# Performance work log

Measured on AMD Instinct MI355X. Metric: run time of the kernel, lower is better.

The kernel has to match this reference:

```python
import jax, jax.numpy as jnp
import numpy as np

CUTOFF = 5.0
N_RBF = 50
N_INTER = 6
B = 1024          # molecules per batch
N_PER_MOL = 32    # atoms per molecule
MAX_Z = 100
D = 128           # n_atom_basis == n_filters == head_hidden


def _ssp(x):
    # schnetpack shifted softplus activation
    return jax.nn.softplus(x) - jnp.log(2.0).astype(x.dtype)


def setup_inputs() -> dict:
    key = jax.random.key(0)
    ks = jax.random.split(key, 18)
    total = B * N_PER_MOL
    atomic_numbers = jax.random.randint(ks[0], (total,), 1, MAX_Z, dtype=jnp.int32)
    positions = jax.random.uniform(ks[1], (total, 3), dtype=jnp.float32) * 10.0
    # all ordered intra-molecule pairs with i != j; pairs beyond the cutoff are
    # zeroed by the cosine cutoff factor, matching the torch neighbor-list math
    loc = np.arange(N_PER_MOL)
    ii, jj = np.meshgrid(loc, loc, indexing='ij')
    m = ii != jj
    li, lj = ii[m], jj[m]                      # [n*(n-1)]
    off = (np.arange(B) * N_PER_MOL)[:, None]
    idx_i = jnp.asarray((off + li[None, :]).reshape(-1), dtype=jnp.int32)
    idx_j = jnp.asarray((off + lj[None, :]).reshape(-1), dtype=jnp.int32)
    batch_idx = jnp.asarray(np.repeat(np.arange(B), N_PER_MOL), dtype=jnp.int32)
    n_atoms = jnp.full((B,), N_PER_MOL, dtype=jnp.int32)
    s = 0.05
    emb = jax.random.normal(ks[2], (MAX_Z, D), jnp.float32) * s
    Wi  = jax.random.normal(ks[3], (N_INTER, D, D), jnp.float32) * s      # in2f (no bias)
    Wf1 = jax.random.normal(ks[4], (N_INTER, N_RBF, D), jnp.float32) * s  # filter net
    bf1 = jax.random.normal(ks[5], (N_INTER, D), jnp.float32) * s
    Wf2 = jax.random.normal(ks[6], (N_INTER, D, D), jnp.float32) * s
    bf2 = jax.random.normal(ks[7], (N_INTER, D), jnp.float32) * s
    Wo1 = jax.random.normal(ks[8], (N_INTER, D, D), jnp.float32) * s      # f2out
    bo1 = jax.random.normal(ks[9], (N_INTER, D), jnp.float32) * s
    Wo2 = jax.random.normal(ks[10], (N_INTER, D, D), jnp.float32) * s
    bo2 = jax.random.normal(ks[11], (N_INTER, D), jnp.float32) * s
    Wh1 = jax.random.normal(ks[12], (D, D), jnp.float32) * s              # MLP head
    bh1 = jax.random.normal(ks[13], (D,), jnp.float32) * s
    Wh2 = jax.random.normal(ks[14], (D, 1), jnp.float32) * s
    bh2 = jax.random.normal(ks[15], (1,), jnp.float32) * s
    return dict(atomic_numbers=atomic_numbers, positions=positions, idx_i=idx_i,
                idx_j=idx_j, batch_idx=batch_idx, n_atoms=n_atoms, emb=emb,
                Wi=Wi, Wf1=Wf1, bf1=bf1, Wf2=Wf2, bf2=bf2,
                Wo1=Wo1, bo1=bo1, Wo2=Wo2, bo2=bo2,
                Wh1=Wh1, bh1=bh1, Wh2=Wh2, bh2=bh2)


def reference(atomic_numbers, positions, idx_i, idx_j, batch_idx, n_atoms,
              emb, Wi, Wf1, bf1, Wf2, bf2, Wo1, bo1, Wo2, bo2,
              Wh1, bh1, Wh2, bh2):
    total = atomic_numbers.shape[0]
    nmol = n_atoms.shape[0]
    # pairwise displacement / distance over neighbor list
    Rij = positions[idx_j] - positions[idx_i]                    # [P,3]
    d = jnp.sqrt(jnp.sum(Rij * Rij, axis=-1))                    # [P]
    # GaussianRBF: centers on [0, cutoff], width = spacing
    centers = jnp.linspace(0.0, CUTOFF, N_RBF, dtype=d.dtype)
    width = CUTOFF / (N_RBF - 1)
    coeff = -0.5 / (width * width)
    f_ij = jnp.exp(coeff * (d[:, None] - centers[None, :]) ** 2)  # [P,R]
    # CosineCutoff (zero beyond cutoff -> out-of-range pairs contribute nothing)
    rcut = 0.5 * (jnp.cos(d * jnp.pi / CUTOFF) + 1.0) * (d < CUTOFF)  # [P]
    x = emb[atomic_numbers]                                       # [N,D]
    for l in range(N_INTER):
        W = _ssp(f_ij @ Wf1[l] + bf1[l]) @ Wf2[l] + bf2[l]        # [P,D] filters
        W = W * rcut[:, None]
        xf = x @ Wi[l]                                            # in2f, no bias
        msg = xf[idx_j] * W                                       # gather + modulate
        agg = jax.ops.segment_sum(msg, idx_i, num_segments=total) # scatter-add
        v = _ssp(agg @ Wo1[l] + bo1[l]) @ Wo2[l] + bo2[l]         # f2out
        x = x + v                                                 # residual
    mol = jax.ops.segment_sum(x, batch_idx, num_segments=nmol)    # sum pooling
    h = jax.nn.silu(mol @ Wh1 + bh1)
    pred = (h @ Wh2 + bh2)[:, 0]                                  # squeeze(-1)
    return pred
```

## Files before the change

kernel.cpp:

```cpp
#include <hip/hip_runtime.h>
#include <math.h>

#define TOTAL  32768
#define NMOL   1024
#define NA     32
#define DIM    128
#define NRBF   50
#define NLAYER 6

typedef __attribute__((ext_vector_type(16))) float f32x16;
typedef _Float16 h2 __attribute__((ext_vector_type(2)));
typedef __fp16 hf8 __attribute__((ext_vector_type(8)));

#define OFF_TAB  0
#define OFF_XBAG 29376
#define OFF_XF   46784
#define OFF_POS  46784
#define OFF_CM   64192
#define LDS_TOTAL 81600

#define WS_WIT   0
#define WS_WO1T  196608
#define WS_WO2T  393216
#define WS_TAB   655360

#define KSTEP  0.10204081632653061f
#define C1     -48.0200005f
#define NTAB   172
#define TSCALE 34.2f

__device__ __forceinline__ unsigned pk2_f16(float lo, float hi) {
  return __builtin_bit_cast(unsigned, __builtin_amdgcn_cvt_pkrtz(lo, hi));
}
__device__ __forceinline__ float ssp_f(float v) {
  float e = __expf(-fabsf(v));
  return fmaxf(v, 0.0f) + __logf(1.0f + e) - 0.69314718055994531f;
}
__device__ __forceinline__ hf8 ldsH(const char* p) {
  return __builtin_bit_cast(hf8, *reinterpret_cast<const uint4*>(p));
}
__device__ __forceinline__ hf8 asH(uint4 u) {
  return __builtin_bit_cast(hf8, u);
}
__device__ __forceinline__ int inv_partner(int r, int i) {
  if (i == 31) return r;
  int mm = i - r; if (mm < 0) mm += 31;
  if (mm == 0) return 31;
  int jj = 2 * r - i; jj %= 31; if (jj < 0) jj += 31;
  return jj;
}

__global__ void k_prep(const float* __restrict__ Wi, const float* __restrict__ Wo1,
                       const float* __restrict__ Wo2, short* __restrict__ ws) {
  const int kind = blockIdx.y, l = blockIdx.z;
  const int idx = blockIdx.x * 256 + threadIdx.x;
  int k = idx >> 7, c = idx & 127;
  const float* s = (kind == 0) ? Wi : (kind == 1) ? Wo1 : Wo2;
  size_t base = (kind == 0) ? WS_WIT : (kind == 1) ? WS_WO1T : WS_WO2T;
  float v = s[(size_t)l * DIM * DIM + k * DIM + c];
  ws[base / 2 + (size_t)l * 16384 + (k >> 3) * 1024 + c * 8 + (k & 7)] =
      (short)__builtin_bit_cast(unsigned short, (_Float16)v);
}

__global__ void k_tab(const float* __restrict__ Wf1, const float* __restrict__ bf1,
                      const float* __restrict__ Wf2, const float* __restrict__ bf2,
                      short* __restrict__ tab) {
  __shared__ float fs[64];
  __shared__ float hs[128];
  const int g = blockIdx.x, l = blockIdx.y, c = threadIdx.x;
  const float d = (float)g * (5.0f / 171.0f);
  if (c < NRBF) { float tt = d - (float)c * KSTEP; fs[c] = __expf(C1 * tt * tt); }
  __syncthreads();
  float h = bf1[l * DIM + c];
#pragma unroll 5
  for (int k = 0; k < NRBF; ++k) h += fs[k] * Wf1[((size_t)l * NRBF + k) * DIM + c];
  hs[c] = ssp_f(h);
  __syncthreads();
  float wv = bf2[l * DIM + c];
#pragma unroll 8
  for (int k = 0; k < DIM; ++k) wv += hs[k] * Wf2[((size_t)l * DIM + k) * DIM + c];
  tab[((size_t)l * NTAB + g) * 136 + c] =
      (short)__builtin_bit_cast(unsigned short, (_Float16)wv);
}

__global__ __launch_bounds__(512, 4) void k_fused(
    const int* __restrict__ z, const float* __restrict__ pos,
    const float* __restrict__ emb,
    const short* __restrict__ wiT, const short* __restrict__ wo1T,
    const short* __restrict__ wo2T, const short* __restrict__ tabA,
    const float* __restrict__ bo1, const float* __restrict__ bo2,
    const float* __restrict__ Wh1, const float* __restrict__ bh1,
    const float* __restrict__ Wh2, const float* __restrict__ bh2,
    float* __restrict__ out) {
  extern __shared__ char sm[];
  const int t = threadIdx.x;
  const int bid = blockIdx.x;
  const int w = t >> 6, lane = t & 63, hl = lane >> 5, lr = lane & 31;
  const int m = w >> 2, wl = w & 3;
  const int ai = t & 31;
  const int acg = (t >> 5) & 7;
  const int cgo = acg * 16;

  char*  XBm = sm + OFF_XBAG + m * 8704;
  char*  AGm = XBm;
  char*  XFm = sm + OFF_XF + m * 8704;
  float* poss = (float*)(sm + OFF_POS);
  const char* CMm = sm + OFF_CM + m * 8704;

  if (t < 192) poss[t] = pos[(size_t)bid * 192 + t];
  __syncthreads();
  for (int u = t; u < 2048; u += 512) {
    int m2 = u >> 10, e = u & 1023;
    int r = e >> 5, i = e & 31;
    uint2 me;
    if (r < 31) {
      int j = inv_partner(r, i);
      const float* pm = poss + m2 * 96;
      float dx = pm[j * 3 + 0] - pm[i * 3 + 0];
      float dy = pm[j * 3 + 1] - pm[i * 3 + 1];
      float dz = pm[j * 3 + 2] - pm[i * 3 + 2];
      float d = sqrtf(dx * dx + dy * dy + dz * dz);
      float rc = 0.5f * (__cosf(d * 0.62831853071795865f) + 1.0f);
      rc = (d < 5.0f) ? rc : 0.0f;
      float u0 = fminf(d * TSCALE, 170.0f);
      int g = (int)u0;
      float f = u0 - (float)g;
      me.x = ((unsigned)(g * 272) << 16) | (unsigned)(j * 272);
      me.y = pk2_f16((1.0f - f) * rc, f * rc);
    } else {
      me.x = 0u; me.y = 0u;
    }
    *(uint2*)(sm + OFF_CM + m2 * 8704 + i * 272 + r * 8) = me;
  }
  float xr[16];
  {
    const float* er = emb + (size_t)z[(bid * 2 + m) * NA + ai] * DIM;
    float4 e0 = *(const float4*)&er[acg * 8];
    float4 e1 = *(const float4*)&er[acg * 8 + 4];
    float4 e2 = *(const float4*)&er[64 + acg * 8];
    float4 e3 = *(const float4*)&er[64 + acg * 8 + 4];
    xr[0] = e0.x; xr[1] = e0.y; xr[2]  = e0.z; xr[3]  = e0.w;
    xr[4] = e1.x; xr[5] = e1.y; xr[6]  = e1.z; xr[7]  = e1.w;
    xr[8] = e2.x; xr[9] = e2.y; xr[10] = e2.z; xr[11] = e2.w;
    xr[12] = e3.x; xr[13] = e3.y; xr[14] = e3.z; xr[15] = e3.w;
  }
  __syncthreads();

  uint4 pt0, pt1, pt2, pt3, pt4, pt5;

  for (int l = 0; l < NLAYER; ++l) {
    const short* wiL  = wiT  + (size_t)l * 16384;
    const short* wo1L = wo1T + (size_t)l * 16384;
    const short* wo2L = wo2T + (size_t)l * 16384;
    const short* tabL = tabA + (size_t)l * NTAB * 136;
    const float bo1r = bo1[l * DIM + wl * 32 + lr];
    const float bo2r = bo2[l * DIM + wl * 32 + lr];
    const int col = wl * 32 + lr;

    if (l > 0) {
      uint4 v0 = *(const uint4*)(XFm + ai * 272 + cgo);
      uint4 v1 = *(const uint4*)(XFm + ai * 272 + cgo + 128);
      h2 hv;
      hv = __builtin_bit_cast(h2, v0.x); xr[0]  += (float)hv[0]; xr[1]  += (float)hv[1];
      hv = __builtin_bit_cast(h2, v0.y); xr[2]  += (float)hv[0]; xr[3]  += (float)hv[1];
      hv = __builtin_bit_cast(h2, v0.z); xr[4]  += (float)hv[0]; xr[5]  += (float)hv[1];
      hv = __builtin_bit_cast(h2, v0.w); xr[6]  += (float)hv[0]; xr[7]  += (float)hv[1];
      hv = __builtin_bit_cast(h2, v1.x); xr[8]  += (float)hv[0]; xr[9]  += (float)hv[1];
      hv = __builtin_bit_cast(h2, v1.y); xr[10] += (float)hv[0]; xr[11] += (float)hv[1];
      hv = __builtin_bit_cast(h2, v1.z); xr[12] += (float)hv[0]; xr[13] += (float)hv[1];
      hv = __builtin_bit_cast(h2, v1.w); xr[14] += (float)hv[0]; xr[15] += (float)hv[1];
    }
    {
      uint4 s0, s1;
      s0.x = pk2_f16(xr[0], xr[1]);   s0.y = pk2_f16(xr[2], xr[3]);
      s0.z = pk2_f16(xr[4], xr[5]);   s0.w = pk2_f16(xr[6], xr[7]);
      s1.x = pk2_f16(xr[8], xr[9]);   s1.y = pk2_f16(xr[10], xr[11]);
      s1.z = pk2_f16(xr[12], xr[13]); s1.w = pk2_f16(xr[14], xr[15]);
      *(uint4*)(XBm + ai * 272 + cgo) = s0;
      *(uint4*)(XBm + ai * 272 + cgo + 128) = s1;
    }
    {
      const uint4* s4 = (const uint4*)tabL;
      pt0 = s4[t]; pt1 = s4[t + 512]; pt2 = s4[t + 1024];
      pt3 = s4[t + 1536]; pt4 = s4[t + 2048];
      if (t < 364) pt5 = s4[t + 2560];
    }
    __syncthreads();

    {
      uint4 bf[8];
#pragma unroll
      for (int ks = 0; ks < 8; ++ks)
        bf[ks] = *(const uint4*)(wiL + (ks * 2 + hl) * 1024 + col * 8);
      f32x16 acc;
#pragma unroll
      for (int q = 0; q < 16; ++q) acc[q] = 0.0f;
#pragma unroll
      for (int ks = 0; ks < 8; ++ks) {
        hf8 a = ldsH(XBm + lr * 272 + ks * 32 + hl * 16);
        acc = __builtin_amdgcn_mfma_f32_32x32x16_f16(a, asH(bf[ks]), acc, 0, 0, 0);
      }
#pragma unroll
      for (int rg = 0; rg < 16; rg += 2) {
        int row = (rg & 3) + 8 * (rg >> 2) + 4 * hl;
        unsigned pk = pk2_f16(acc[rg], acc[rg + 1]);
        *(unsigned short*)(XFm + row * 272 + col * 2) = (unsigned short)pk;
        *(unsigned short*)(XFm + (row + 1) * 272 + col * 2) = (unsigned short)(pk >> 16);
      }
    }
    __syncthreads();

    ((uint4*)(sm + OFF_TAB))[t] = pt0;
    ((uint4*)(sm + OFF_TAB))[t + 512] = pt1;
    ((uint4*)(sm + OFF_TAB))[t + 1024] = pt2;
    ((uint4*)(sm + OFF_TAB))[t + 1536] = pt3;
    ((uint4*)(sm + OFF_TAB))[t + 2048] = pt4;
    if (t < 364) ((uint4*)(sm + OFF_TAB))[t + 2560] = pt5;
    __syncthreads();

    h2 acc_h[8];
#pragma unroll
    for (int q = 0; q < 8; ++q) acc_h[q] = (h2)(_Float16)0.0f;
#pragma unroll 2
    for (int k = 0; k < 16; ++k) {
      uint4 ME = *(const uint4*)(CMm + ai * 272 + k * 16);
#define AGROUND(mex, mey)                                                 \
      {                                                                   \
        int foff = (int)((mex) & 0xFFFFu);                                \
        int gboff = (int)((mex) >> 16);                                   \
        unsigned a = (mey);                                               \
        h2 a00h = __builtin_bit_cast(h2, __builtin_amdgcn_perm(a, a, 0x01000100u)); \
        h2 a11h = __builtin_bit_cast(h2, __builtin_amdgcn_perm(a, a, 0x03020302u)); \
        const char* tp = sm + OFF_TAB + gboff + cgo;                      \
        uint4 T00 = *(const uint4*)(tp);                                  \
        uint4 T01 = *(const uint4*)(tp + 128);                            \
        uint4 T10 = *(const uint4*)(tp + 272);                            \
        uint4 T11 = *(const uint4*)(tp + 400);                            \
        const char* fp = XFm + foff + cgo;                                \
        uint4 F0 = *(const uint4*)(fp);                                   \
        uint4 F1 = *(const uint4*)(fp + 128);                             \
        h2 wv;                                                            \
        wv = a00h * __builtin_bit_cast(h2, T00.x) + a11h * __builtin_bit_cast(h2, T10.x); \
        acc_h[0] = wv * __builtin_bit_cast(h2, F0.x) + acc_h[0];          \
        wv = a00h * __builtin_bit_cast(h2, T00.y) + a11h * __builtin_bit_cast(h2, T10.y); \
        acc_h[1] = wv * __builtin_bit_cast(h2, F0.y) + acc_h[1];          \
        wv = a00h * __builtin_bit_cast(h2, T00.z) + a11h * __builtin_bit_cast(h2, T10.z); \
        acc_h[2] = wv * __builtin_bit_cast(h2, F0.z) + acc_h[2];          \
        wv = a00h * __builtin_bit_cast(h2, T00.w) + a11h * __builtin_bit_cast(h2, T10.w); \
        acc_h[3] = wv * __builtin_bit_cast(h2, F0.w) + acc_h[3];          \
        wv = a00h * __builtin_bit_cast(h2, T01.x) + a11h * __builtin_bit_cast(h2, T11.x); \
        acc_h[4] = wv * __builtin_bit_cast(h2, F1.x) + acc_h[4];          \
        wv = a00h * __builtin_bit_cast(h2, T01.y) + a11h * __builtin_bit_cast(h2, T11.y); \
        acc_h[5] = wv * __builtin_bit_cast(h2, F1.y) + acc_h[5];          \
        wv = a00h * __builtin_bit_cast(h2, T01.z) + a11h * __builtin_bit_cast(h2, T11.z); \
        acc_h[6] = wv * __builtin_bit_cast(h2, F1.z) + acc_h[6];          \
        wv = a00h * __builtin_bit_cast(h2, T01.w) + a11h * __builtin_bit_cast(h2, T11.w); \
        acc_h[7] = wv * __builtin_bit_cast(h2, F1.w) + acc_h[7];          \
      }
      AGROUND(ME.x, ME.y)
      AGROUND(ME.z, ME.w)
#undef AGROUND
    }
    __syncthreads();

    {
      uint4 s0, s1;
      s0.x = __builtin_bit_cast(unsigned, acc_h[0]);
      s0.y = __builtin_bit_cast(unsigned, acc_h[1]);
      s0.z = __builtin_bit_cast(unsigned, acc_h[2]);
      s0.w = __builtin_bit_cast(unsigned, acc_h[3]);
      s1.x = __builtin_bit_cast(unsigned, acc_h[4]);
      s1.y = __builtin_bit_cast(unsigned, acc_h[5]);
      s1.z = __builtin_bit_cast(unsigned, acc_h[6]);
      s1.w = __builtin_bit_cast(unsigned, acc_h[7]);
      *(uint4*)(AGm + ai * 272 + cgo) = s0;
      *(uint4*)(AGm + ai * 272 + cgo + 128) = s1;
    }
    __syncthreads();

    float t1v[16];
    {
      uint4 bf[8];
#pragma unroll
      for (int ks = 0; ks < 8; ++ks)
        bf[ks] = *(const uint4*)(wo1L + (ks * 2 + hl) * 1024 + col * 8);
      f32x16 acc;
#pragma unroll
      for (int q = 0; q < 16; ++q) acc[q] = 0.0f;
#pragma unroll
      for (int ks = 0; ks < 8; ++ks) {
        hf8 a = ldsH(AGm + lr * 272 + ks * 32 + hl * 16);
        acc = __builtin_amdgcn_mfma_f32_32x32x16_f16(a, asH(bf[ks]), acc, 0, 0, 0);
      }
#pragma unroll
      for (int rg = 0; rg < 16; ++rg) t1v[rg] = ssp_f(acc[rg] + bo1r);
    }
    __syncthreads();

    {
#pragma unroll
      for (int rg = 0; rg < 16; rg += 2) {
        int row = (rg & 3) + 8 * (rg >> 2) + 4 * hl;
        unsigned pk = pk2_f16(t1v[rg], t1v[rg + 1]);
        *(unsigned short*)(AGm + row * 272 + col * 2) = (unsigned short)pk;
        *(unsigned short*)(AGm + (row + 1) * 272 + col * 2) = (unsigned short)(pk >> 16);
      }
    }
    __syncthreads();

    {
      uint4 bf[8];
#pragma unroll
      for (int ks = 0; ks < 8; ++ks)
        bf[ks] = *(const uint4*)(wo2L + (ks * 2 + hl) * 1024 + col * 8);
      f32x16 acc;
#pragma unroll
      for (int q = 0; q < 16; ++q) acc[q] = 0.0f;
#pragma unroll
      for (int ks = 0; ks < 8; ++ks) {
        hf8 a = ldsH(AGm + lr * 272 + ks * 32 + hl * 16);
        acc = __builtin_amdgcn_mfma_f32_32x32x16_f16(a, asH(bf[ks]), acc, 0, 0, 0);
      }
#pragma unroll
      for (int rg = 0; rg < 16; rg += 2) {
        int row = (rg & 3) + 8 * (rg >> 2) + 4 * hl;
        unsigned pk = pk2_f16(acc[rg] + bo2r, acc[rg + 1] + bo2r);
        *(unsigned short*)(XFm + row * 272 + col * 2) = (unsigned short)pk;
        *(unsigned short*)(XFm + (row + 1) * 272 + col * 2) = (unsigned short)(pk >> 16);
      }
    }
    __syncthreads();
  }

  {
    uint4 v0 = *(const uint4*)(XFm + ai * 272 + cgo);
    uint4 v1 = *(const uint4*)(XFm + ai * 272 + cgo + 128);
    h2 hv;
    hv = __builtin_bit_cast(h2, v0.x); xr[0]  += (float)hv[0]; xr[1]  += (float)hv[1];
    hv = __builtin_bit_cast(h2, v0.y); xr[2]  += (float)hv[0]; xr[3]  += (float)hv[1];
    hv = __builtin_bit_cast(h2, v0.z); xr[4]  += (float)hv[0]; xr[5]  += (float)hv[1];
    hv = __builtin_bit_cast(h2, v0.w); xr[6]  += (float)hv[0]; xr[7]  += (float)hv[1];
    hv = __builtin_bit_cast(h2, v1.x); xr[8]  += (float)hv[0]; xr[9]  += (float)hv[1];
    hv = __builtin_bit_cast(h2, v1.y); xr[10] += (float)hv[0]; xr[11] += (float)hv[1];
    hv = __builtin_bit_cast(h2, v1.z); xr[12] += (float)hv[0]; xr[13] += (float)hv[1];
    hv = __builtin_bit_cast(h2, v1.w); xr[14] += (float)hv[0]; xr[15] += (float)hv[1];
  }

#pragma unroll
  for (int off = 1; off < 32; off <<= 1) {
#pragma unroll
    for (int q = 0; q < 16; ++q) xr[q] += __shfl_xor(xr[q], off);
  }
  float* molS = (float*)(sm + 0);
  float* hsum = (float*)(sm + 2048);
  if (ai == 0) {
#pragma unroll
    for (int q = 0; q < 8; ++q) molS[m * 132 + acg * 8 + q] = xr[q];
#pragma unroll
    for (int q = 0; q < 8; ++q) molS[m * 132 + 64 + acg * 8 + q] = xr[8 + q];
  }
  __syncthreads();
  if (t < 256) {
    int mm = t >> 7, c = t & 127;
    float h = bh1[c];
#pragma unroll 8
    for (int k = 0; k < 128; ++k) h += molS[mm * 132 + k] * Wh1[k * 128 + c];
    h = h / (1.0f + __expf(-h));
    hsum[mm * 128 + c] = h * Wh2[c];
  }
  for (int off = 64; off > 0; off >>= 1) {
    __syncthreads();
    if (t < 256) {
      int mm = t >> 7, c = t & 127;
      if (c < off) hsum[mm * 128 + c] += hsum[mm * 128 + c + off];
    }
  }
  __syncthreads();
  if (t < 2) out[bid * 2 + t] = hsum[t * 128] + bh2[0];
}

extern "C" void kernel_launch(void* const* d_in, const int* in_sizes, int n_in,
                              void* d_out, int out_size, void* d_ws, size_t ws_size,
                              hipStream_t stream) {
  const int*   z    = (const int*)d_in[0];
  const float* pos  = (const float*)d_in[1];
  const float* emb  = (const float*)d_in[6];
  const float* Wi   = (const float*)d_in[7];
  const float* Wf1  = (const float*)d_in[8];
  const float* bf1  = (const float*)d_in[9];
  const float* Wf2  = (const float*)d_in[10];
  const float* bf2  = (const float*)d_in[11];
  const float* Wo1  = (const float*)d_in[12];
  const float* bo1  = (const float*)d_in[13];
  const float* Wo2  = (const float*)d_in[14];
  const float* bo2  = (const float*)d_in[15];
  const float* Wh1  = (const float*)d_in[16];
  const float* bh1  = (const float*)d_in[17];
  const float* Wh2  = (const float*)d_in[18];
  const float* bh2  = (const float*)d_in[19];
  float* out = (float*)d_out;

  short* wsS = (short*)d_ws;
  const short* wiT  = wsS + WS_WIT  / 2;
  const short* wo1T = wsS + WS_WO1T / 2;
  const short* wo2T = wsS + WS_WO2T / 2;
  const short* tab  = wsS + WS_TAB  / 2;

  (void)hipFuncSetAttribute(reinterpret_cast<const void*>(k_fused),
                            hipFuncAttributeMaxDynamicSharedMemorySize, LDS_TOTAL);

  k_prep<<<dim3(64, 3, 6), 256, 0, stream>>>(Wi, Wo1, Wo2, wsS);
  k_tab<<<dim3(NTAB, 6), 128, 0, stream>>>(Wf1, bf1, Wf2, bf2, wsS + WS_TAB / 2);
  k_fused<<<NMOL / 2, 512, LDS_TOTAL, stream>>>(
      z, pos, emb, wiT, wo1T, wo2T, tab, bo1, bo2, Wh1, bh1, Wh2, bh2, out);
}
```

Measured before the change: 118.4 us.

## Compact per-atom neighbor lists to in-cutoff pairs and bound aggregation loop

Builds a compacted per-atom list holding only neighbor pairs with distance below the cutoff, zero-padded to 32 entries. A wave-level max reduction stores the padded maximum neighbor count per molecule in spare row padding. The message aggregation loop in every layer then runs only to that count instead of over all 31 partners. This skips filter and gather work for pairs the cosine cutoff would zero anyway, at the cost of a serial 31-step list build done by only 64 threads and a data-dependent trip count.

```diff
diff --git a/kernel.cpp b/kernel.cpp
--- a/kernel.cpp
+++ b/kernel.cpp
@@ -109,28 +109,35 @@
 
   if (t < 192) poss[t] = pos[(size_t)bid * 192 + t];
   __syncthreads();
-  for (int u = t; u < 2048; u += 512) {
-    int m2 = u >> 10, e = u & 1023;
-    int r = e >> 5, i = e & 31;
-    uint2 me;
-    if (r < 31) {
+  if (t < 64) {
+    const int m2 = t >> 5, i = t & 31;
+    const float* pm = poss + m2 * 96;
+    const float xi = pm[i * 3 + 0], yi = pm[i * 3 + 1], zi = pm[i * 3 + 2];
+    char* row = sm + OFF_CM + m2 * 8704 + i * 272;
+    int n = 0;
+    for (int r = 0; r < 31; ++r) {
       int j = inv_partner(r, i);
-      const float* pm = poss + m2 * 96;
-      float dx = pm[j * 3 + 0] - pm[i * 3 + 0];
-      float dy = pm[j * 3 + 1] - pm[i * 3 + 1];
-      float dz = pm[j * 3 + 2] - pm[i * 3 + 2];
+      float dx = pm[j * 3 + 0] - xi;
+      float dy = pm[j * 3 + 1] - yi;
+      float dz = pm[j * 3 + 2] - zi;
       float d = sqrtf(dx * dx + dy * dy + dz * dz);
-      float rc = 0.5f * (__cosf(d * 0.62831853071795865f) + 1.0f);
-      rc = (d < 5.0f) ? rc : 0.0f;
-      float u0 = fminf(d * TSCALE, 170.0f);
-      int g = (int)u0;
-      float f = u0 - (float)g;
-      me.x = ((unsigned)(g * 272) << 16) | (unsigned)(j * 272);
-      me.y = pk2_f16((1.0f - f) * rc, f * rc);
-    } else {
-      me.x = 0u; me.y = 0u;
-    }
-    *(uint2*)(sm + OFF_CM + m2 * 8704 + i * 272 + r * 8) = me;
+      if (d < 5.0f) {
+        float rc = 0.5f * (__cosf(d * 0.62831853071795865f) + 1.0f);
+        float u0 = fminf(d * TSCALE, 170.0f);
+        int g = (int)u0;
+        float f = u0 - (float)g;
+        uint2 me;
+        me.x = ((unsigned)(g * 272) << 16) | (unsigned)(j * 272);
+        me.y = pk2_f16((1.0f - f) * rc, f * rc);
+        *(uint2*)(row + n * 8) = me;
+        ++n;
+      }
+    }
+    for (int s = n; s < 32; ++s) { uint2 zz; zz.x = 0u; zz.y = 0u; *(uint2*)(row + s * 8) = zz; }
+    int mx = n;
+#pragma unroll
+    for (int off = 1; off < 32; off <<= 1) mx = max(mx, __shfl_xor(mx, off));
+    if ((t & 31) == 0) *(int*)(sm + OFF_CM + m2 * 8704 + 256) = (mx + 1) & ~1;
   }
   float xr[16];
   {
@@ -145,6 +152,8 @@
     xr[12] = e3.x; xr[13] = e3.y; xr[14] = e3.z; xr[15] = e3.w;
   }
   __syncthreads();
+
+  const int nmax = *(const int*)(CMm + 256);
 
   uint4 pt0, pt1, pt2, pt3, pt4, pt5;
 
@@ -221,9 +230,8 @@
     h2 acc_h[8];
 #pragma unroll
     for (int q = 0; q < 8; ++q) acc_h[q] = (h2)(_Float16)0.0f;
-#pragma unroll 2
-    for (int k = 0; k < 16; ++k) {
-      uint4 ME = *(const uint4*)(CMm + ai * 272 + k * 16);
+    for (int k = 0; k < nmax; k += 2) {
+      uint4 ME = *(const uint4*)(CMm + ai * 272 + k * 8);
 #define AGROUND(mex, mey)                                                 \
       {                                                                   \
         int foff = (int)((mex) & 0xFFFFu);                                \
```

Measured after the change: 109.8 us. 1.08x faster.
